# Kernel tuning notes

Measured on AMD Instinct MI355X. Metric: run time of the kernel, lower is better.

## Reference

```python
import jax, jax.numpy as jnp
import numpy as np

N = 50000; E = 800000; T = 800000; G = 64
H = 128; IEMB = 128; BAS = 8; NS = 4; NR = 6; OEH = 128; OUT = 1; NB = 4; CUT = 5.0


def envelope(x):
    # exponent=5 -> p=6: 1/x + a*x^5 + b*x^6 + c*x^7 with a=-28, b=48, c=-21
    return 1.0 / x - 28.0 * x**5 + 48.0 * x**6 - 21.0 * x**7


def setup_inputs() -> dict:
    key = jax.random.key(0)
    ks = iter(jax.random.split(key, 80))
    def w(shape, s=0.1):
        return jax.random.normal(next(ks), shape, dtype=jnp.float32) * s
    inp = {}
    inp['z'] = jax.random.randint(next(ks), (N,), 0, 100, dtype=jnp.int32)
    inp['dist'] = jax.random.uniform(next(ks), (E,), jnp.float32, 0.05, 1.0)
    inp['dist_trip'] = jax.random.uniform(next(ks), (T,), jnp.float32, 0.05, 1.0)
    inp['angle'] = jax.random.uniform(next(ks), (T,), jnp.float32, -1.0, 1.0)
    inp['edge_index'] = jax.random.randint(next(ks), (2, E), 0, N, dtype=jnp.int32)
    inp['triplets'] = jax.random.randint(next(ks), (T, 3), 0, N, dtype=jnp.int32)
    inp['batch'] = jnp.sort(jax.random.randint(next(ks), (N,), 0, G, dtype=jnp.int32))
    inp['atom_table'] = w((100, H), 1.0)
    inp['rbf_freq'] = jnp.arange(1, NR + 1, dtype=jnp.float32) * jnp.float32(np.pi)
    inp['sbf_freq'] = jnp.arange(1, NR + 1, dtype=jnp.float32) * jnp.float32(np.pi)
    inp['emb_w1'] = w((NR, IEMB)); inp['emb_b1'] = w((IEMB,), 0.01)
    inp['emb_w2'] = w((IEMB, H)); inp['emb_b2'] = w((H,), 0.01)
    inp['iw_rbf1'] = w((NB, NR, BAS)); inp['iw_rbf2'] = w((NB, BAS, H))
    inp['iw_sbf1'] = w((NB, NS * NR, BAS)); inp['iw_sbf2'] = w((NB, BAS, IEMB))
    inp['iw_t1'] = w((NB, H, IEMB)); inp['iw_t2'] = w((NB, IEMB, H)); inp['ib_t2'] = w((NB, H), 0.01)
    inp['iw_up'] = w((NB, H, H)); inp['ib_up'] = w((NB, H), 0.01)
    inp['iw_down'] = w((NB, H, H)); inp['ib_down'] = w((NB, H), 0.01)
    inp['ow_rbf'] = w((NB + 1, NR, H))
    inp['ow0'] = w((NB + 1, H, OEH)); inp['ob0'] = w((NB + 1, OEH), 0.01)
    inp['ow1'] = w((NB + 1, OEH, OEH)); inp['ob1'] = w((NB + 1, OEH), 0.01)
    inp['ow2'] = w((NB + 1, OEH, OUT)); inp['ob2'] = w((NB + 1, OUT), 0.01)
    return inp


def _forward(atom_table, rbf_freq, sbf_freq, emb_w1, emb_b1, emb_w2, emb_b2,
             iw_rbf1, iw_rbf2, iw_sbf1, iw_sbf2, iw_t1, iw_t2, ib_t2,
             iw_up, ib_up, iw_down, ib_down, ow_rbf, ow0, ob0, ow1, ob1, ow2, ob2,
             dist, dist_trip, angle, z, edge_index, triplets, batch):
    row, col = edge_index[0], edge_index[1]
    j_idx = triplets[:, 1]
    # radial basis for edges: [E, NR]
    d = dist[:, None] / CUT
    rbf_e = envelope(d) * jnp.sin(rbf_freq * d)
    # spherical basis for triplets: [T, NS*NR]
    dt = dist_trip[:, None] / CUT
    rbf_t = envelope(dt) * jnp.sin(sbf_freq * dt)
    a = angle[:, None]
    sph = jnp.concatenate([jnp.ones_like(a), a, 0.5 * (3 * a**2 - 1), 0.5 * (5 * a**3 - 3 * a)], axis=-1)
    sbf_t = (rbf_t[:, None, :] * sph[:, :, None]).reshape(a.shape[0], -1)

    x = atom_table[z]  # [N, H]
    # EmbeddingBlock: edge msg from rbf only, scattered to col
    e = jax.nn.silu(rbf_e @ emb_w1 + emb_b1) @ emb_w2 + emb_b2
    x = x + jax.ops.segment_sum(e, col, num_segments=N)

    def out_block(k, x):
        rbf_emb = rbf_e @ ow_rbf[k]            # [E, H]
        h = jax.ops.segment_sum(x[row] * rbf_emb, col, num_segments=N)
        h = jax.nn.silu(h @ ow0[k] + ob0[k])
        h = jax.nn.silu(h @ ow1[k] + ob1[k])
        return h @ ow2[k] + ob2[k]             # [N, OUT]

    P = out_block(0, x)
    for b in range(NB):
        x_up = x @ iw_up[b] + ib_up[b]
        x_down = x @ iw_down[b] + ib_down[b]
        rbf_emb = jax.nn.silu(rbf_e @ iw_rbf1[b]) @ iw_rbf2[b]      # [E, H]
        x_edge = x_up[row] * rbf_emb                                  # [E, H]
        sbf_emb = jax.nn.silu(sbf_t @ iw_sbf1[b]) @ iw_sbf2[b]      # [T, H]
        t = jax.nn.silu(x_down @ iw_t1[b]) @ iw_t2[b] + ib_t2[b]     # [N, H]
        # original: for each triplet i, x_edge += t[j]*sbf_emb[i] (broadcast over all edges)
        extra = jnp.sum(t[j_idx] * sbf_emb, axis=0)                   # [H]
        x_edge = x_edge + extra
        x = x + jax.ops.segment_sum(x_edge, col, num_segments=N)
        P = P + out_block(b + 1, x)

    counts = jax.ops.segment_sum(jnp.ones((x.shape[0],), jnp.float32), batch, num_segments=G)
    pooled = jax.ops.segment_sum(P, batch, num_segments=G) / jnp.maximum(counts, 1.0)[:, None]
    return pooled  # [G, OUT]


def reference(z, dist, dist_trip, angle, edge_index, triplets, batch, atom_table, rbf_freq, sbf_freq,
              emb_w1, emb_b1, emb_w2, emb_b2, iw_rbf1, iw_rbf2, iw_sbf1, iw_sbf2, iw_t1, iw_t2, ib_t2,
              iw_up, ib_up, iw_down, ib_down, ow_rbf, ow0, ob0, ow1, ob1, ow2, ob2):
    return _forward(atom_table, rbf_freq, sbf_freq, emb_w1, emb_b1, emb_w2, emb_b2,
                    iw_rbf1, iw_rbf2, iw_sbf1, iw_sbf2, iw_t1, iw_t2, ib_t2,
                    iw_up, ib_up, iw_down, ib_down, ow_rbf, ow0, ob0, ow1, ob1, ow2, ob2,
                    dist, dist_trip, angle, z, edge_index, triplets, batch)
```

## Files before the change

kernel.cpp:

```cpp
#include <hip/hip_runtime.h>
#include <hip/hip_fp16.h>

#define N_ 50000
#define E_ 800000
#define T_ 800000
#define G_ 64
#define H_ 128

#define NBK 782
#define NSB (NBK * 8)
#define CAPS 512

typedef __attribute__((ext_vector_type(8))) short bf16x8;
typedef __attribute__((ext_vector_type(4))) float f32x4;
typedef _Float16 f16x2 __attribute__((ext_vector_type(2)));

__device__ __forceinline__ float siluf(float v) {
    return __fdividef(v, 1.0f + __expf(-v));
}

__device__ __forceinline__ unsigned short f2bf(float f) {
    unsigned int u = __float_as_uint(f);
    u += 0x7fffu + ((u >> 16) & 1u);
    return (unsigned short)(u >> 16);
}
__device__ __forceinline__ unsigned int f2bf2(float a, float b) {
    return (unsigned int)f2bf(a) | ((unsigned int)f2bf(b) << 16);
}
__device__ __forceinline__ float bf2f(unsigned short h) {
    return __uint_as_float(((unsigned int)h) << 16);
}
__device__ __forceinline__ float2 bf2x2(unsigned int p) {
    return make_float2(__uint_as_float(p << 16), __uint_as_float(p & 0xffff0000u));
}
__device__ __forceinline__ float fdot2f(f16x2 a, f16x2 b, float c) {
    return __builtin_amdgcn_fdot2(a, b, c, false);
}

__global__ __launch_bounds__(256) void k_bucket(const int* __restrict__ ecol,
                                                const int* __restrict__ trip,
                                                int* bcntE, unsigned int* __restrict__ ebkt, int* __restrict__ degE,
                                                int* bcntT, unsigned int* __restrict__ tbkt, int* __restrict__ degT) {
    int i = blockIdx.x * 256 + threadIdx.x;
    int r = blockIdx.x & 7;
    if (i < E_) {
        int col = ecol[i];
        int sb = (col >> 6) * 8 + r;
        int pos = atomicAdd(&bcntE[sb], 1);
        if (pos < CAPS) {
            ebkt[(size_t)sb * CAPS + pos] = ((unsigned int)i << 6) | (unsigned int)(col & 63);
            atomicAdd(&degE[col], 1);
        }
    }
    int t = i - E_;
    if (t >= 0 && t < T_) {
        int j = trip[3 * t + 1];
        int sb = (j >> 6) * 8 + r;
        int pos = atomicAdd(&bcntT[sb], 1);
        if (pos < CAPS) {
            tbkt[(size_t)sb * CAPS + pos] = ((unsigned int)t << 6) | (unsigned int)(j & 63);
            atomicAdd(&degT[j], 1);
        }
    }
}

__global__ __launch_bounds__(1024) void k_scan2(const int* __restrict__ degE, int* rowptrE, int* curE,
                                                const int* __restrict__ degT, int* rowptrT, int* curT, int n) {
    const int* deg = (blockIdx.x == 0) ? degE : degT;
    int* rowptr = (blockIdx.x == 0) ? rowptrE : rowptrT;
    int* cur = (blockIdx.x == 0) ? curE : curT;
    __shared__ int wsum[16];
    __shared__ int s_carry;
    int tid = threadIdx.x, lane = tid & 63, w = tid >> 6;
    if (tid == 0) s_carry = 0;
    __syncthreads();
    for (int base = 0; base < n; base += 1024) {
        int i = base + tid;
        int v = (i < n) ? deg[i] : 0;
        int incl = v;
        #pragma unroll
        for (int s = 1; s < 64; s <<= 1) {
            int t = __shfl_up(incl, (unsigned)s, 64);
            if (lane >= s) incl += t;
        }
        if (lane == 63) wsum[w] = incl;
        __syncthreads();
        int carry0 = s_carry;
        int wexcl = 0;
        for (int j = 0; j < w; ++j) wexcl += wsum[j];
        int excl = carry0 + wexcl + (incl - v);
        if (i < n) { rowptr[i] = excl; cur[i] = excl; }
        __syncthreads();
        if (tid == 1023) s_carry = carry0 + wexcl + incl;
        __syncthreads();
    }
    if (tid == 0) rowptr[n] = s_carry;
}

__global__ __launch_bounds__(256) void k_place(const int* __restrict__ bcntE, const unsigned int* __restrict__ ebkt,
                                               const int* __restrict__ erow, const float* __restrict__ dist,
                                               int* curE, int* __restrict__ slist, float* __restrict__ distS,
                                               const int* __restrict__ bcntT, const unsigned int* __restrict__ tbkt,
                                               const float* __restrict__ dist_trip, const float* __restrict__ angle,
                                               int* curT, float2* __restrict__ tpay) {
    int b = blockIdx.x;
    bool isE = b < NBK;
    if (!isE) b -= NBK;
    int tid = threadIdx.x;
    if (isE) {
        for (int s = 0; s < 8; ++s) {
            int sb = b * 8 + s;
            int nb = min(bcntE[sb], CAPS);
            for (int i = tid; i < nb; i += 256) {
                unsigned int rec = ebkt[(size_t)sb * CAPS + i];
                int e = (int)(rec >> 6);
                int col = b * 64 + (int)(rec & 63u);
                int pos = atomicAdd(&curE[col], 1);
                slist[pos] = erow[e];
                distS[pos] = dist[e];
            }
        }
    } else {
        for (int s = 0; s < 8; ++s) {
            int sb = b * 8 + s;
            int nb = min(bcntT[sb], CAPS);
            for (int i = tid; i < nb; i += 256) {
                unsigned int rec = tbkt[(size_t)sb * CAPS + i];
                int t = (int)(rec >> 6);
                int col = b * 64 + (int)(rec & 63u);
                int pos = atomicAdd(&curT[col], 1);
                tpay[pos] = make_float2(dist_trip[t], angle[t]);
            }
        }
    }
}

__global__ __launch_bounds__(256) void k_wprep(const float* __restrict__ emb_w2, const float* __restrict__ iw_down,
                                               const float* __restrict__ iw_t1, const float* __restrict__ iw_t2,
                                               const float* __restrict__ iw_up, const float* __restrict__ ow0,
                                               const float* __restrict__ ow1, unsigned short* __restrict__ Wt) {
    int mat = blockIdx.x >> 3;
    int part = blockIdx.x & 7;
    const float* src;
    if (mat == 0) src = emb_w2;
    else if (mat < 5) src = iw_down + (size_t)(mat - 1) * 16384;
    else if (mat < 9) src = iw_t1 + (size_t)(mat - 5) * 16384;
    else if (mat < 13) src = iw_t2 + (size_t)(mat - 9) * 16384;
    else if (mat < 17) src = iw_up + (size_t)(mat - 13) * 16384;
    else if (mat < 22) src = ow0 + (size_t)(mat - 17) * 16384;
    else src = ow1 + (size_t)(mat - 22) * 16384;
    unsigned short* dst = Wt + (size_t)mat * 16384;
    int base = part * 2048;
    for (int i = base + threadIdx.x; i < base + 2048; i += 256) {
        int k = i >> 7, n = i & 127;
        dst[n * 128 + k] = f2bf(src[i]);
    }
}

__global__ __launch_bounds__(256) void k_geom(const float* __restrict__ distS,
                                              const float* __restrict__ freq, const float* __restrict__ iw_rbf1,
                                              float* __restrict__ rbfS, __half* __restrict__ s8all, int n) {
    __shared__ float W1s[4][48];
    int tid = threadIdx.x;
    if (tid < 192) W1s[tid / 48][tid % 48] = iw_rbf1[tid];
    __syncthreads();
    int p = blockIdx.x * 256 + tid;
    if (p >= n) return;
    float d = distS[p] * 0.2f;
    float d2 = d * d, d4 = d2 * d2, d5 = d4 * d;
    float env = __fdividef(1.0f, d) - 28.0f * d5 + 48.0f * d5 * d - 21.0f * d5 * d2;
    float rb[6];
    #pragma unroll
    for (int r = 0; r < 6; ++r) {
        rb[r] = env * __sinf(freq[r] * d);
        rbfS[(size_t)p * 6 + r] = rb[r];
    }
    #pragma unroll
    for (int b = 0; b < 4; ++b) {
        __half out[8];
        #pragma unroll
        for (int k = 0; k < 8; ++k) {
            float u = 0.f;
            #pragma unroll
            for (int r = 0; r < 6; ++r) u += rb[r] * W1s[b][r * 8 + k];
            out[k] = __float2half(siluf(u));
        }
        *(uint4*)&s8all[((size_t)b * n + p) * 8] = *(uint4*)out;
    }
}

__global__ __launch_bounds__(256) void k_basis(const float2* __restrict__ tpay,
                                               const float* __restrict__ sfreq, __half* __restrict__ basis, int n) {
    int t = blockIdx.x * 256 + threadIdx.x;
    if (t >= n) return;
    float2 da = tpay[t];
    float d = da.x * 0.2f;
    float a = da.y;
    float d2 = d * d, d4 = d2 * d2, d5 = d4 * d;
    float env = __fdividef(1.0f, d) - 28.0f * d5 + 48.0f * d5 * d - 21.0f * d5 * d2;
    float rb[6];
    #pragma unroll
    for (int r = 0; r < 6; ++r) rb[r] = env * __sinf(sfreq[r] * d);
    float sph[4];
    sph[0] = 1.0f; sph[1] = a; sph[2] = 1.5f * a * a - 0.5f; sph[3] = 2.5f * a * a * a - 1.5f * a;
    __half out[24];
    #pragma unroll
    for (int s = 0; s < 4; ++s)
        #pragma unroll
        for (int r = 0; r < 6; ++r) out[s * 6 + r] = __float2half(sph[s] * rb[r]);
    uint4* dst = (uint4*)(basis + (size_t)t * 24);
    dst[0] = ((uint4*)out)[0];
    dst[1] = ((uint4*)out)[1];
    dst[2] = ((uint4*)out)[2];
}

__global__ __launch_bounds__(256) void k_sv4(const int* __restrict__ rowptrT, const __half* __restrict__ basis,
                                             const float* __restrict__ iw_sbf1, float* __restrict__ SV4, int n) {
    int wave = threadIdx.x >> 6, lane = threadIdx.x & 63;
    int node = blockIdx.x * 8 + wave * 2 + (lane >> 5);
    int sub = lane & 31;
    int blk = sub >> 3, k = sub & 7;
    if (node >= n) return;
    const float* W1 = iw_sbf1 + blk * 192;
    f16x2 w[12];
    #pragma unroll
    for (int j = 0; j < 12; ++j) {
        f16x2 t;
        t.x = (_Float16)W1[(2 * j) * 8 + k];
        t.y = (_Float16)W1[(2 * j + 1) * 8 + k];
        w[j] = t;
    }
    float acc = 0.f;
    int p0 = rowptrT[node], p1 = rowptrT[node + 1];
    for (int p = p0; p < p1; ++p) {
        union { uint4 q[3]; f16x2 h[12]; } bs;
        const uint4* bp = (const uint4*)(basis + (size_t)p * 24);
        bs.q[0] = bp[0]; bs.q[1] = bp[1]; bs.q[2] = bp[2];
        float u = 0.f;
        #pragma unroll
        for (int j = 0; j < 12; ++j) u = fdot2f(bs.h[j], w[j], u);
        acc += siluf(u);
    }
    SV4[((size_t)blk * n + node) * 8 + k] = acc;
}

__global__ __launch_bounds__(256) void k_init_x(const float* __restrict__ atab, const int* __restrict__ z,
                                                unsigned short* __restrict__ xh, int n) {
    int t = blockIdx.x * 256 + threadIdx.x;
    if (t >= n * 16) return;
    int node = t >> 4, q = t & 15;
    const float4* a4 = (const float4*)atab;
    float4 v0 = a4[(size_t)z[node] * 32 + q * 2];
    float4 v1 = a4[(size_t)z[node] * 32 + q * 2 + 1];
    uint4 pk;
    pk.x = f2bf2(v0.x, v0.y);
    pk.y = f2bf2(v0.z, v0.w);
    pk.z = f2bf2(v1.x, v1.y);
    pk.w = f2bf2(v1.z, v1.w);
    ((uint4*)xh)[t] = pk;
}

__global__ __launch_bounds__(256) void k_embS(const int* __restrict__ rowptr, const float* __restrict__ rbfS,
                                              const float* __restrict__ w1, const float* __restrict__ b1,
                                              unsigned short* __restrict__ SSh, int n) {
    int node = blockIdx.x * 4 + (threadIdx.x >> 6);
    int lane = threadIdx.x & 63;
    if (node >= n) return;
    int c = lane * 2;
    float wc0[6], wc1[6];
    #pragma unroll
    for (int r = 0; r < 6; ++r) { wc0[r] = w1[r * 128 + c]; wc1[r] = w1[r * 128 + c + 1]; }
    float bb0 = b1[c], bb1 = b1[c + 1];
    float a0 = 0.f, a1 = 0.f;
    int p0 = rowptr[node], p1 = rowptr[node + 1];
    for (int p = p0; p < p1; ++p) {
        const float2* r2 = (const float2*)&rbfS[(size_t)p * 6];
        float2 ra = r2[0], rbx = r2[1], rc = r2[2];
        float u0 = bb0 + ra.x * wc0[0] + ra.y * wc0[1] + rbx.x * wc0[2] + rbx.y * wc0[3] + rc.x * wc0[4] + rc.y * wc0[5];
        float u1 = bb1 + ra.x * wc1[0] + ra.y * wc1[1] + rbx.x * wc1[2] + rbx.y * wc1[3] + rc.x * wc1[4] + rc.y * wc1[5];
        a0 += siluf(u0);
        a1 += siluf(u1);
    }
    *(unsigned int*)&SSh[(size_t)node * 128 + c] = f2bf2(a0, a1);
}

template <int BIAS_MODE, bool SILU, bool ACCBF, bool ABF, bool WF32, bool WBF>
__global__ __launch_bounds__(256, 4) void k_gemm_mfma(const void* __restrict__ Ap,
                                                      const unsigned short* __restrict__ Wt,
                                                      const float* __restrict__ bias, const int* __restrict__ deg,
                                                      float* __restrict__ C, unsigned short* __restrict__ Ch, int M) {
    int tid = threadIdx.x;
    int wave = tid >> 6, lane = tid & 63;
    int m15 = lane & 15, quad = lane >> 4;
    int row0 = blockIdx.x * 64 + wave * 16;
    int arow = row0 + m15;
    if (arow > M - 1) arow = M - 1;

    f32x4 acc[8];
    #pragma unroll
    for (int nt = 0; nt < 8; ++nt) acc[nt] = (f32x4){0.f, 0.f, 0.f, 0.f};

    #pragma unroll
    for (int kt = 0; kt < 4; ++kt) {
        int ks = kt * 32 + quad * 8;
        bf16x8 av;
        if constexpr (ABF) {
            av = *(const bf16x8*)((const unsigned short*)Ap + (size_t)arow * 128 + ks);
        } else {
            const float* Arow = (const float*)Ap + (size_t)arow * 128;
            float4 a0 = *(const float4*)(Arow + ks);
            float4 a1 = *(const float4*)(Arow + ks + 4);
            union { bf16x8 v; unsigned int u[4]; } af;
            af.u[0] = f2bf2(a0.x, a0.y);
            af.u[1] = f2bf2(a0.z, a0.w);
            af.u[2] = f2bf2(a1.x, a1.y);
            af.u[3] = f2bf2(a1.z, a1.w);
            av = af.v;
        }
        #pragma unroll
        for (int nt = 0; nt < 8; ++nt) {
            bf16x8 bf = *(const bf16x8*)(Wt + (size_t)(nt * 16 + m15) * 128 + ks);
            acc[nt] = __builtin_amdgcn_mfma_f32_16x16x32_bf16(av, bf, acc[nt], 0, 0, 0);
        }
    }

    #pragma unroll
    for (int nt = 0; nt < 8; ++nt) {
        int col = nt * 16 + m15;
        float bc = 0.f;
        if constexpr (BIAS_MODE != 0) bc = bias[col];
        #pragma unroll
        for (int reg = 0; reg < 4; ++reg) {
            int row = row0 + quad * 4 + reg;
            if (row < M) {
                float v = acc[nt][reg];
                if constexpr (BIAS_MODE == 1) v += bc;
                if constexpr (BIAS_MODE == 2) v += bc * (float)deg[row];
                if constexpr (SILU) v = siluf(v);
                if constexpr (ACCBF) v += bf2f(Ch[(size_t)row * 128 + col]);
                if constexpr (WF32) C[(size_t)row * 128 + col] = v;
                if constexpr (WBF) Ch[(size_t)row * 128 + col] = f2bf(v);
            }
        }
    }
}

template <int PACC>
__global__ __launch_bounds__(256, 4) void k_out_mlp(const unsigned short* __restrict__ hB,
                                                    const unsigned short* __restrict__ W0t, const float* __restrict__ b0,
                                                    const unsigned short* __restrict__ W1t, const float* __restrict__ b1,
                                                    const float* __restrict__ w2col, const float* __restrict__ ob2p,
                                                    float* __restrict__ Pout, int M) {
    __shared__ unsigned short lds[4][16 * 136];
    int tid = threadIdx.x;
    int wave = tid >> 6, lane = tid & 63;
    int m15 = lane & 15, quad = lane >> 4;
    int row0 = blockIdx.x * 64 + wave * 16;
    int arow = row0 + m15;
    if (arow > M - 1) arow = M - 1;
    unsigned short* L = lds[wave];

    f32x4 acc[8];
    #pragma unroll
    for (int nt = 0; nt < 8; ++nt) acc[nt] = (f32x4){0.f, 0.f, 0.f, 0.f};
    #pragma unroll
    for (int kt = 0; kt < 4; ++kt) {
        int ks = kt * 32 + quad * 8;
        bf16x8 av = *(const bf16x8*)(hB + (size_t)arow * 128 + ks);
        #pragma unroll
        for (int nt = 0; nt < 8; ++nt) {
            bf16x8 bf = *(const bf16x8*)(W0t + (size_t)(nt * 16 + m15) * 128 + ks);
            acc[nt] = __builtin_amdgcn_mfma_f32_16x16x32_bf16(av, bf, acc[nt], 0, 0, 0);
        }
    }
    #pragma unroll
    for (int nt = 0; nt < 8; ++nt) {
        int col = nt * 16 + m15;
        float bc = b0[col];
        #pragma unroll
        for (int reg = 0; reg < 4; ++reg)
            L[(quad * 4 + reg) * 136 + col] = f2bf(siluf(acc[nt][reg] + bc));
    }
    __syncthreads();

    #pragma unroll
    for (int nt = 0; nt < 8; ++nt) acc[nt] = (f32x4){0.f, 0.f, 0.f, 0.f};
    #pragma unroll
    for (int kt = 0; kt < 4; ++kt) {
        int ks = kt * 32 + quad * 8;
        bf16x8 av = *(const bf16x8*)(L + m15 * 136 + ks);
        #pragma unroll
        for (int nt = 0; nt < 8; ++nt) {
            bf16x8 bf = *(const bf16x8*)(W1t + (size_t)(nt * 16 + m15) * 128 + ks);
            acc[nt] = __builtin_amdgcn_mfma_f32_16x16x32_bf16(av, bf, acc[nt], 0, 0, 0);
        }
    }
    float w2c[8], pp[4];
    #pragma unroll
    for (int nt = 0; nt < 8; ++nt) w2c[nt] = w2col[nt * 16 + m15];
    #pragma unroll
    for (int reg = 0; reg < 4; ++reg) pp[reg] = 0.f;
    #pragma unroll
    for (int nt = 0; nt < 8; ++nt) {
        float bc = b1[nt * 16 + m15];
        #pragma unroll
        for (int reg = 0; reg < 4; ++reg)
            pp[reg] += siluf(acc[nt][reg] + bc) * w2c[nt];
    }
    #pragma unroll
    for (int reg = 0; reg < 4; ++reg) {
        float s = pp[reg];
        s += __shfl_xor(s, 1, 64);
        s += __shfl_xor(s, 2, 64);
        s += __shfl_xor(s, 4, 64);
        s += __shfl_xor(s, 8, 64);
        if (m15 == 0) {
            int row = row0 + quad * 4 + reg;
            if (row < M) {
                float r = s + ob2p[0];
                if constexpr (PACC == 2) r += Pout[row];
                Pout[row] = r;
            }
        }
    }
}

__global__ __launch_bounds__(256, 4) void k_block_mlp(const unsigned short* __restrict__ xh,
                                                      const unsigned short* __restrict__ Wd, const float* __restrict__ bd,
                                                      const unsigned short* __restrict__ Wt1,
                                                      const unsigned short* __restrict__ Wt2, const float* __restrict__ bt2,
                                                      const unsigned short* __restrict__ Wup, const float* __restrict__ bup,
                                                      const float* __restrict__ SV, const float* __restrict__ W2,
                                                      float* __restrict__ extra,
                                                      unsigned short* __restrict__ xuph, int M) {
    __shared__ union {
        unsigned short h[4][16 * 136];
        float f[64 * 132];
    } sm;
    int tid = threadIdx.x;
    int wave = tid >> 6, lane = tid & 63;
    int m15 = lane & 15, quad = lane >> 4;
    int row0 = blockIdx.x * 64 + wave * 16;
    int arow = row0 + m15;
    if (arow > M - 1) arow = M - 1;
    unsigned short* L = sm.h[wave];

    f32x4 accD[8], accU[8];
    #pragma unroll
    for (int nt = 0; nt < 8; ++nt) { accD[nt] = (f32x4){0.f, 0.f, 0.f, 0.f}; accU[nt] = (f32x4){0.f, 0.f, 0.f, 0.f}; }
    #pragma unroll
    for (int kt = 0; kt < 4; ++kt) {
        int ks = kt * 32 + quad * 8;
        bf16x8 av = *(const bf16x8*)(xh + (size_t)arow * 128 + ks);
        #pragma unroll
        for (int nt = 0; nt < 8; ++nt) {
            bf16x8 bd_ = *(const bf16x8*)(Wd + (size_t)(nt * 16 + m15) * 128 + ks);
            accD[nt] = __builtin_amdgcn_mfma_f32_16x16x32_bf16(av, bd_, accD[nt], 0, 0, 0);
            bf16x8 bu_ = *(const bf16x8*)(Wup + (size_t)(nt * 16 + m15) * 128 + ks);
            accU[nt] = __builtin_amdgcn_mfma_f32_16x16x32_bf16(av, bu_, accU[nt], 0, 0, 0);
        }
    }
    #pragma unroll
    for (int nt = 0; nt < 8; ++nt) {
        int col = nt * 16 + m15;
        float bcu = bup[col], bcd = bd[col];
        #pragma unroll
        for (int reg = 0; reg < 4; ++reg) {
            int row = row0 + quad * 4 + reg;
            if (row < M) xuph[(size_t)row * 128 + col] = f2bf(accU[nt][reg] + bcu);
            L[(quad * 4 + reg) * 136 + col] = f2bf(accD[nt][reg] + bcd);
        }
    }
    __syncthreads();

    #pragma unroll
    for (int nt = 0; nt < 8; ++nt) accD[nt] = (f32x4){0.f, 0.f, 0.f, 0.f};
    #pragma unroll
    for (int kt = 0; kt < 4; ++kt) {
        int ks = kt * 32 + quad * 8;
        bf16x8 av = *(const bf16x8*)(L + m15 * 136 + ks);
        #pragma unroll
        for (int nt = 0; nt < 8; ++nt) {
            bf16x8 bf = *(const bf16x8*)(Wt1 + (size_t)(nt * 16 + m15) * 128 + ks);
            accD[nt] = __builtin_amdgcn_mfma_f32_16x16x32_bf16(av, bf, accD[nt], 0, 0, 0);
        }
    }
    __syncthreads();
    #pragma unroll
    for (int nt = 0; nt < 8; ++nt) {
        int col = nt * 16 + m15;
        #pragma unroll
        for (int reg = 0; reg < 4; ++reg)
            L[(quad * 4 + reg) * 136 + col] = f2bf(siluf(accD[nt][reg]));
    }
    __syncthreads();

    #pragma unroll
    for (int nt = 0; nt < 8; ++nt) accD[nt] = (f32x4){0.f, 0.f, 0.f, 0.f};
    #pragma unroll
    for (int kt = 0; kt < 4; ++kt) {
        int ks = kt * 32 + quad * 8;
        bf16x8 av = *(const bf16x8*)(L + m15 * 136 + ks);
        #pragma unroll
        for (int nt = 0; nt < 8; ++nt) {
            bf16x8 bf = *(const bf16x8*)(Wt2 + (size_t)(nt * 16 + m15) * 128 + ks);
            accD[nt] = __builtin_amdgcn_mfma_f32_16x16x32_bf16(av, bf, accD[nt], 0, 0, 0);
        }
    }
    __syncthreads();
    #pragma unroll
    for (int nt = 0; nt < 8; ++nt) {
        int col = nt * 16 + m15;
        float bc = bt2[col];
        #pragma unroll
        for (int reg = 0; reg < 4; ++reg) {
            int lr = wave * 16 + quad * 4 + reg;
            sm.f[lr * 132 + col] = accD[nt][reg] + bc;
        }
    }
    __syncthreads();

    int col = tid & 127, half = tid >> 7;
    float acc8[8];
    #pragma unroll
    for (int k = 0; k < 8; ++k) acc8[k] = 0.f;
    int rmax = M - blockIdx.x * 64;
    if (rmax > 64) rmax = 64;
    for (int rr = half; rr < rmax; rr += 2) {
        float t = sm.f[rr * 132 + col];
        const float4* sv4 = (const float4*)&SV[(size_t)(blockIdx.x * 64 + rr) * 8];
        float4 s0 = sv4[0], s1 = sv4[1];
        acc8[0] += t * s0.x; acc8[1] += t * s0.y; acc8[2] += t * s0.z; acc8[3] += t * s0.w;
        acc8[4] += t * s1.x; acc8[5] += t * s1.y; acc8[6] += t * s1.z; acc8[7] += t * s1.w;
    }
    float e = 0.f;
    #pragma unroll
    for (int k = 0; k < 8; ++k) e += acc8[k] * W2[k * 128 + col];
    __syncthreads();
    sm.f[tid] = e;
    __syncthreads();
    if (tid < 128) atomicAdd(&extra[col], sm.f[tid] + sm.f[tid + 128]);
}

__global__ __launch_bounds__(256) void k_out_gather(const int* __restrict__ rowptr, const int* __restrict__ slist,
                                                    const float* __restrict__ rbfS,
                                                    const unsigned short* __restrict__ xh,
                                                    const float* __restrict__ wrbf,
                                                    unsigned short* __restrict__ hB, int n) {
    int node = blockIdx.x * 4 + (threadIdx.x >> 6);
    int lane = threadIdx.x & 63;
    if (node >= n) return;
    int c = lane * 2;
    float wc0[6], wc1[6];
    #pragma unroll
    for (int r = 0; r < 6; ++r) { wc0[r] = wrbf[r * 128 + c]; wc1[r] = wrbf[r * 128 + c + 1]; }
    float a0 = 0.f, a1 = 0.f;
    int p0 = rowptr[node], p1 = rowptr[node + 1];
    int p = p0;
    for (; p + 4 <= p1; p += 4) {
        int s0 = slist[p], s1 = slist[p + 1], s2 = slist[p + 2], s3 = slist[p + 3];
        float2 rb[4][3];
        #pragma unroll
        for (int u = 0; u < 4; ++u) {
            const float2* r2 = (const float2*)&rbfS[(size_t)(p + u) * 6];
            rb[u][0] = r2[0]; rb[u][1] = r2[1]; rb[u][2] = r2[2];
        }
        unsigned int xv0 = *(const unsigned int*)&xh[(size_t)s0 * 128 + c];
        unsigned int xv1 = *(const unsigned int*)&xh[(size_t)s1 * 128 + c];
        unsigned int xv2 = *(const unsigned int*)&xh[(size_t)s2 * 128 + c];
        unsigned int xv3 = *(const unsigned int*)&xh[(size_t)s3 * 128 + c];
        #pragma unroll
        for (int u = 0; u < 4; ++u) {
            float e0 = rb[u][0].x * wc0[0] + rb[u][0].y * wc0[1] + rb[u][1].x * wc0[2] +
                       rb[u][1].y * wc0[3] + rb[u][2].x * wc0[4] + rb[u][2].y * wc0[5];
            float e1 = rb[u][0].x * wc1[0] + rb[u][0].y * wc1[1] + rb[u][1].x * wc1[2] +
                       rb[u][1].y * wc1[3] + rb[u][2].x * wc1[4] + rb[u][2].y * wc1[5];
            float2 xf = bf2x2((u == 0) ? xv0 : (u == 1) ? xv1 : (u == 2) ? xv2 : xv3);
            a0 += xf.x * e0;
            a1 += xf.y * e1;
        }
    }
    for (; p < p1; ++p) {
        int src = slist[p];
        const float2* r2 = (const float2*)&rbfS[(size_t)p * 6];
        float2 ra = r2[0], rbx = r2[1], rc = r2[2];
        float e0 = ra.x * wc0[0] + ra.y * wc0[1] + rbx.x * wc0[2] + rbx.y * wc0[3] + rc.x * wc0[4] + rc.y * wc0[5];
        float e1 = ra.x * wc1[0] + ra.y * wc1[1] + rbx.x * wc1[2] + rbx.y * wc1[3] + rc.x * wc1[4] + rc.y * wc1[5];
        float2 xf = bf2x2(*(const unsigned int*)&xh[(size_t)src * 128 + c]);
        a0 += xf.x * e0;
        a1 += xf.y * e1;
    }
    *(unsigned int*)&hB[(size_t)node * 128 + c] = f2bf2(a0, a1);
}

__global__ __launch_bounds__(256) void k_interact(const int* __restrict__ rowptr, const int* __restrict__ slist,
                                                  const __half* __restrict__ s8, const float* __restrict__ W2,
                                                  const float* __restrict__ extra,
                                                  const unsigned short* __restrict__ xuph,
                                                  unsigned short* __restrict__ xh, int n) {
    int node = blockIdx.x * 4 + (threadIdx.x >> 6);
    int lane = threadIdx.x & 63;
    if (node >= n) return;
    int c = lane * 2;
    f16x2 w2a[4], w2b[4];
    #pragma unroll
    for (int j = 0; j < 4; ++j) {
        f16x2 wa, wb;
        wa.x = (_Float16)W2[(2 * j) * 128 + c];
        wa.y = (_Float16)W2[(2 * j + 1) * 128 + c];
        wb.x = (_Float16)W2[(2 * j) * 128 + c + 1];
        wb.y = (_Float16)W2[(2 * j + 1) * 128 + c + 1];
        w2a[j] = wa;
        w2b[j] = wb;
    }
    int p0 = rowptr[node], p1 = rowptr[node + 1];
    float cntf = (float)(p1 - p0);
    float a0 = cntf * extra[c], a1 = cntf * extra[c + 1];
    int p = p0;
    for (; p + 4 <= p1; p += 4) {
        int s0 = slist[p], s1 = slist[p + 1], s2 = slist[p + 2], s3 = slist[p + 3];
        uint4 sv[4];
        #pragma unroll
        for (int u = 0; u < 4; ++u) sv[u] = *(const uint4*)(s8 + (size_t)(p + u) * 8);
        unsigned int xv0 = *(const unsigned int*)&xuph[(size_t)s0 * 128 + c];
        unsigned int xv1 = *(const unsigned int*)&xuph[(size_t)s1 * 128 + c];
        unsigned int xv2 = *(const unsigned int*)&xuph[(size_t)s2 * 128 + c];
        unsigned int xv3 = *(const unsigned int*)&xuph[(size_t)s3 * 128 + c];
        #pragma unroll
        for (int u = 0; u < 4; ++u) {
            union { uint4 q; f16x2 h[4]; } s;
            s.q = sv[u];
            float e0 = fdot2f(s.h[0], w2a[0], 0.f);
            e0 = fdot2f(s.h[1], w2a[1], e0);
            e0 = fdot2f(s.h[2], w2a[2], e0);
            e0 = fdot2f(s.h[3], w2a[3], e0);
            float e1 = fdot2f(s.h[0], w2b[0], 0.f);
            e1 = fdot2f(s.h[1], w2b[1], e1);
            e1 = fdot2f(s.h[2], w2b[2], e1);
            e1 = fdot2f(s.h[3], w2b[3], e1);
            float2 xf = bf2x2((u == 0) ? xv0 : (u == 1) ? xv1 : (u == 2) ? xv2 : xv3);
            a0 += xf.x * e0;
            a1 += xf.y * e1;
        }
    }
    for (; p < p1; ++p) {
        int src = slist[p];
        float2 xf = bf2x2(*(const unsigned int*)&xuph[(size_t)src * 128 + c]);
        union { uint4 q; f16x2 h[4]; } s;
        s.q = *(const uint4*)(s8 + (size_t)p * 8);
        float e0 = fdot2f(s.h[0], w2a[0], 0.f);
        e0 = fdot2f(s.h[1], w2a[1], e0);
        e0 = fdot2f(s.h[2], w2a[2], e0);
        e0 = fdot2f(s.h[3], w2a[3], e0);
        float e1 = fdot2f(s.h[0], w2b[0], 0.f);
        e1 = fdot2f(s.h[1], w2b[1], e1);
        e1 = fdot2f(s.h[2], w2b[2], e1);
        e1 = fdot2f(s.h[3], w2b[3], e1);
        a0 += xf.x * e0;
        a1 += xf.y * e1;
    }
    unsigned int cur = *(unsigned int*)&xh[(size_t)node * 128 + c];
    float2 xc = bf2x2(cur);
    *(unsigned int*)&xh[(size_t)node * 128 + c] = f2bf2(xc.x + a0, xc.y + a1);
}

__global__ __launch_bounds__(256) void k_pool(const float* __restrict__ P, const int* __restrict__ batch,
                                              float* __restrict__ pool, float* __restrict__ cnt, int n) {
    int i = blockIdx.x * 256 + threadIdx.x;
    int lane = threadIdx.x & 63;
    int b = (i < n) ? batch[i] : -1;
    float p = (i < n) ? P[i] : 0.f;
    int b0 = __shfl(b, 0, 64);
    int b63 = __shfl(b, 63, 64);
    if (b0 == b63 && b0 >= 0) {
        float s = p;
        #pragma unroll
        for (int off = 32; off > 0; off >>= 1) s += __shfl_xor(s, off, 64);
        if (lane == 0) {
            atomicAdd(&pool[b0], s);
            atomicAdd(&cnt[b0], 64.0f);
        }
    } else {
        if (i < n) {
            atomicAdd(&pool[b], p);
            atomicAdd(&cnt[b], 1.0f);
        }
    }
}

__global__ __launch_bounds__(64) void k_final(const float* __restrict__ pool, const float* __restrict__ cnt,
                                              float* __restrict__ out) {
    int g = threadIdx.x;
    if (g < G_) out[g] = __fdividef(pool[g], fmaxf(cnt[g], 1.0f));
}

extern "C" void kernel_launch(void* const* d_in, const int* in_sizes, int n_in,
                              void* d_out, int out_size, void* d_ws, size_t ws_size,
                              hipStream_t stream) {
    (void)in_sizes; (void)n_in; (void)out_size; (void)ws_size;
    const int* z = (const int*)d_in[0];
    const float* dist = (const float*)d_in[1];
    const float* dist_trip = (const float*)d_in[2];
    const float* angle = (const float*)d_in[3];
    const int* edge_index = (const int*)d_in[4];
    const int* triplets = (const int*)d_in[5];
    const int* batch = (const int*)d_in[6];
    const float* atom_table = (const float*)d_in[7];
    const float* rbf_freq = (const float*)d_in[8];
    const float* sbf_freq = (const float*)d_in[9];
    const float* emb_w1 = (const float*)d_in[10];
    const float* emb_b1 = (const float*)d_in[11];
    const float* emb_w2 = (const float*)d_in[12];
    const float* emb_b2 = (const float*)d_in[13];
    const float* iw_rbf1 = (const float*)d_in[14];
    const float* iw_rbf2 = (const float*)d_in[15];
    const float* iw_sbf1 = (const float*)d_in[16];
    const float* iw_sbf2 = (const float*)d_in[17];
    const float* iw_t1 = (const float*)d_in[18];
    const float* iw_t2 = (const float*)d_in[19];
    const float* ib_t2 = (const float*)d_in[20];
    const float* iw_up = (const float*)d_in[21];
    const float* ib_up = (const float*)d_in[22];
    const float* iw_down = (const float*)d_in[23];
    const float* ib_down = (const float*)d_in[24];
    const float* ow_rbf = (const float*)d_in[25];
    const float* ow0 = (const float*)d_in[26];
    const float* ob0 = (const float*)d_in[27];
    const float* ow1 = (const float*)d_in[28];
    const float* ob1 = (const float*)d_in[29];
    const float* ow2 = (const float*)d_in[30];
    const float* ob2 = (const float*)d_in[31];

    const int* erow = edge_index;
    const int* ecol = edge_index + E_;

    float* ws = (float*)d_ws;
    float* bufA = ws;
    float* bufB = bufA + (size_t)N_ * H_;
    float* P = bufB + (size_t)N_ * H_;
    float* rbfS = P + N_;
    float* SV4 = rbfS + (size_t)E_ * 6;
    float* extra4 = SV4 + (size_t)4 * N_ * 8;
    float* pool = extra4 + 512;
    float* cnt = pool + G_;
    int* bcntE = (int*)(cnt + G_);
    int* bcntT = bcntE + NSB;
    int* degE = bcntT + NSB;
    int* degT = degE + N_;
    int* rowptr = degT + N_;
    int* curE = rowptr + N_ + 1;
    int* curT = curE + N_;
    int* slist = curT + N_;
    int* rowptrT = slist + E_;
    float* distS = (float*)(rowptrT + N_ + 1);
    uintptr_t tp = (uintptr_t)(distS + E_);
    tp = (tp + 7) & ~(uintptr_t)7;
    float2* tpay = (float2*)tp;
    __half* s8all = (__half*)(tpay + T_);
    __half* basis = s8all + (size_t)4 * E_ * 8;
    unsigned short* xh = (unsigned short*)(basis + (size_t)T_ * 24);
    unsigned short* xuph = xh + (size_t)N_ * H_;
    unsigned short* Wt = xuph + (size_t)N_ * H_;
    unsigned short* hB = (unsigned short*)bufB;

    unsigned int* ebkt = (unsigned int*)s8all;
    unsigned int* tbkt = ebkt + (size_t)NSB * CAPS;

    const int EG = (E_ + 255) / 256;
    const int TG = (T_ + 255) / 256;
    const int ETG = (E_ + T_ + 255) / 256;
    const int NG4 = (N_ + 3) / 4;
    const int GEMMG = (N_ + 63) / 64;

    hipMemsetAsync(extra4, 0, (512 + 2 * G_ + 2 * NSB + 2 * N_) * sizeof(float), stream);
    k_wprep<<<27 * 8, 256, 0, stream>>>(emb_w2, iw_down, iw_t1, iw_t2, iw_up, ow0, ow1, Wt);
    k_bucket<<<ETG, 256, 0, stream>>>(ecol, triplets, bcntE, ebkt, degE, bcntT, tbkt, degT);
    k_scan2<<<2, 1024, 0, stream>>>(degE, rowptr, curE, degT, rowptrT, curT, N_);
    k_place<<<2 * NBK, 256, 0, stream>>>(bcntE, ebkt, erow, dist, curE, slist, distS,
                                         bcntT, tbkt, dist_trip, angle, curT, tpay);

    k_geom<<<EG, 256, 0, stream>>>(distS, rbf_freq, iw_rbf1, rbfS, s8all, E_);
    k_basis<<<TG, 256, 0, stream>>>(tpay, sbf_freq, basis, T_);
    k_sv4<<<(N_ + 7) / 8, 256, 0, stream>>>(rowptrT, basis, iw_sbf1, SV4, N_);
    k_init_x<<<(N_ * 16 + 255) / 256, 256, 0, stream>>>(atom_table, z, xh, N_);

    k_embS<<<NG4, 256, 0, stream>>>(rowptr, rbfS, emb_w1, emb_b1, (unsigned short*)bufA, N_);
    k_gemm_mfma<2, false, true, true, false, true><<<GEMMG, 256, 0, stream>>>(
        bufA, Wt, emb_b2, degE, nullptr, xh, N_);

    auto out_block = [&](int k, bool first) {
        k_out_gather<<<NG4, 256, 0, stream>>>(rowptr, slist, rbfS, xh,
                                              ow_rbf + (size_t)k * 6 * 128, hB, N_);
        if (first)
            k_out_mlp<1><<<GEMMG, 256, 0, stream>>>(hB, Wt + (size_t)(17 + k) * 16384, ob0 + k * 128,
                                                    Wt + (size_t)(22 + k) * 16384, ob1 + k * 128,
                                                    ow2 + k * 128, ob2 + k, P, N_);
        else
            k_out_mlp<2><<<GEMMG, 256, 0, stream>>>(hB, Wt + (size_t)(17 + k) * 16384, ob0 + k * 128,
                                                    Wt + (size_t)(22 + k) * 16384, ob1 + k * 128,
                                                    ow2 + k * 128, ob2 + k, P, N_);
    };

    out_block(0, true);

    for (int b = 0; b < 4; ++b) {
        k_block_mlp<<<GEMMG, 256, 0, stream>>>(xh,
                                               Wt + (size_t)(1 + b) * 16384, ib_down + b * 128,
                                               Wt + (size_t)(5 + b) * 16384,
                                               Wt + (size_t)(9 + b) * 16384, ib_t2 + b * 128,
                                               Wt + (size_t)(13 + b) * 16384, ib_up + b * 128,
                                               SV4 + (size_t)b * N_ * 8,
                                               iw_sbf2 + (size_t)b * 1024,
                                               extra4 + b * 128,
                                               xuph, N_);
        k_interact<<<NG4, 256, 0, stream>>>(rowptr, slist, s8all + (size_t)b * E_ * 8,
                                            iw_rbf2 + (size_t)b * 1024, extra4 + b * 128,
                                            xuph, xh, N_);
        out_block(b + 1, false);
    }

    k_pool<<<(N_ + 255) / 256, 256, 0, stream>>>(P, batch, pool, cnt, N_);
    k_final<<<1, 64, 0, stream>>>(pool, cnt, (float*)d_out);
}
```

Baseline: 1.701 ms.

## Rebuild CSR construction with block-local histograms and per-bucket scans

The bucketing kernel now gives each block a 4096-element chunk and builds a shared-memory histogram per bucket, so each block issues one global atomic per bucket instead of one per element. The global per-node degree count and the 50k-element serial scan are replaced by a small scan over 782 bucket totals. The place kernel then computes per-column offsets in shared memory and writes rowptr itself, and the GEMM derives degree from rowptr differences. This cuts global atomic traffic and the long single-block scan, at the cost of extra LDS atomics and a second pass over the buckets in place.

Measured after the change: 1.508 ms. -11.4%, faster.

```diff
diff --git a/kernel.cpp b/kernel.cpp
--- a/kernel.cpp
+++ b/kernel.cpp
@@ -10,6 +10,9 @@
 #define NBK 782
 #define NSB (NBK * 8)
 #define CAPS 512
+#define CHUNK 4096
+#define EB ((E_ + CHUNK - 1) / CHUNK)
+#define TB ((T_ + CHUNK - 1) / CHUNK)
 
 typedef __attribute__((ext_vector_type(8))) short bf16x8;
 typedef __attribute__((ext_vector_type(4))) float f32x4;
@@ -39,97 +42,137 @@
 
 __global__ __launch_bounds__(256) void k_bucket(const int* __restrict__ ecol,
                                                 const int* __restrict__ trip,
-                                                int* bcntE, unsigned int* __restrict__ ebkt, int* __restrict__ degE,
-                                                int* bcntT, unsigned int* __restrict__ tbkt, int* __restrict__ degT) {
-    int i = blockIdx.x * 256 + threadIdx.x;
-    int r = blockIdx.x & 7;
-    if (i < E_) {
-        int col = ecol[i];
-        int sb = (col >> 6) * 8 + r;
-        int pos = atomicAdd(&bcntE[sb], 1);
-        if (pos < CAPS) {
-            ebkt[(size_t)sb * CAPS + pos] = ((unsigned int)i << 6) | (unsigned int)(col & 63);
-            atomicAdd(&degE[col], 1);
-        }
-    }
-    int t = i - E_;
-    if (t >= 0 && t < T_) {
-        int j = trip[3 * t + 1];
-        int sb = (j >> 6) * 8 + r;
-        int pos = atomicAdd(&bcntT[sb], 1);
-        if (pos < CAPS) {
-            tbkt[(size_t)sb * CAPS + pos] = ((unsigned int)t << 6) | (unsigned int)(j & 63);
-            atomicAdd(&degT[j], 1);
-        }
-    }
-}
-
-__global__ __launch_bounds__(1024) void k_scan2(const int* __restrict__ degE, int* rowptrE, int* curE,
-                                                const int* __restrict__ degT, int* rowptrT, int* curT, int n) {
-    const int* deg = (blockIdx.x == 0) ? degE : degT;
-    int* rowptr = (blockIdx.x == 0) ? rowptrE : rowptrT;
-    int* cur = (blockIdx.x == 0) ? curE : curT;
+                                                int* bcntE, unsigned int* __restrict__ ebkt,
+                                                int* bcntT, unsigned int* __restrict__ tbkt) {
+    __shared__ int hist[NBK];
+    __shared__ int bbase[NBK];
+    int blk = blockIdx.x;
+    bool isE = blk < EB;
+    int ebase = (isE ? blk : blk - EB) * CHUNK;
+    const int nElem = isE ? E_ : T_;
+    int r = blk & 7;
+    int* bcnt = isE ? bcntE : bcntT;
+    unsigned int* bkt = isE ? ebkt : tbkt;
+    int tid = threadIdx.x;
+
+    for (int i = tid; i < NBK; i += 256) hist[i] = 0;
+    __syncthreads();
+
+    int cols[16];
+    #pragma unroll
+    for (int u = 0; u < 16; ++u) {
+        int idx = ebase + u * 256 + tid;
+        int c = -1;
+        if (idx < nElem) c = isE ? ecol[idx] : trip[3 * idx + 1];
+        cols[u] = c;
+        if (c >= 0) atomicAdd(&hist[c >> 6], 1);
+    }
+    __syncthreads();
+
+    for (int b = tid; b < NBK; b += 256) {
+        int c = hist[b];
+        bbase[b] = c ? atomicAdd(&bcnt[b * 8 + r], c) : 0;
+        hist[b] = 0;
+    }
+    __syncthreads();
+
+    #pragma unroll
+    for (int u = 0; u < 16; ++u) {
+        int c = cols[u];
+        if (c >= 0) {
+            int bk = c >> 6;
+            int off = atomicAdd(&hist[bk], 1);
+            int pos = bbase[bk] + off;
+            if (pos < CAPS) {
+                int idx = ebase + u * 256 + tid;
+                bkt[(size_t)(bk * 8 + r) * CAPS + pos] =
+                    ((unsigned int)idx << 6) | (unsigned int)(c & 63);
+            }
+        }
+    }
+}
+
+__global__ __launch_bounds__(1024) void k_scanB(const int* __restrict__ bcntE, int* bktbaseE,
+                                                const int* __restrict__ bcntT, int* bktbaseT) {
+    const int* bcnt = (blockIdx.x == 0) ? bcntE : bcntT;
+    int* bb = (blockIdx.x == 0) ? bktbaseE : bktbaseT;
+    int tid = threadIdx.x, lane = tid & 63, w = tid >> 6;
     __shared__ int wsum[16];
-    __shared__ int s_carry;
-    int tid = threadIdx.x, lane = tid & 63, w = tid >> 6;
-    if (tid == 0) s_carry = 0;
-    __syncthreads();
-    for (int base = 0; base < n; base += 1024) {
-        int i = base + tid;
-        int v = (i < n) ? deg[i] : 0;
-        int incl = v;
-        #pragma unroll
-        for (int s = 1; s < 64; s <<= 1) {
-            int t = __shfl_up(incl, (unsigned)s, 64);
-            if (lane >= s) incl += t;
-        }
-        if (lane == 63) wsum[w] = incl;
-        __syncthreads();
-        int carry0 = s_carry;
-        int wexcl = 0;
-        for (int j = 0; j < w; ++j) wexcl += wsum[j];
-        int excl = carry0 + wexcl + (incl - v);
-        if (i < n) { rowptr[i] = excl; cur[i] = excl; }
-        __syncthreads();
-        if (tid == 1023) s_carry = carry0 + wexcl + incl;
-        __syncthreads();
-    }
-    if (tid == 0) rowptr[n] = s_carry;
+    int v = 0;
+    if (tid < NBK) {
+        #pragma unroll
+        for (int s = 0; s < 8; ++s) v += min(bcnt[tid * 8 + s], CAPS);
+    }
+    int incl = v;
+    #pragma unroll
+    for (int s = 1; s < 64; s <<= 1) {
+        int t = __shfl_up(incl, (unsigned)s, 64);
+        if (lane >= s) incl += t;
+    }
+    if (lane == 63) wsum[w] = incl;
+    __syncthreads();
+    int wexcl = 0;
+    for (int j = 0; j < w; ++j) wexcl += wsum[j];
+    if (tid < NBK) bb[tid] = wexcl + incl - v;
 }
 
 __global__ __launch_bounds__(256) void k_place(const int* __restrict__ bcntE, const unsigned int* __restrict__ ebkt,
                                                const int* __restrict__ erow, const float* __restrict__ dist,
-                                               int* curE, int* __restrict__ slist, float* __restrict__ distS,
+                                               const int* __restrict__ bktbaseE, int* __restrict__ rowptrE,
+                                               int* __restrict__ slist, float* __restrict__ distS,
                                                const int* __restrict__ bcntT, const unsigned int* __restrict__ tbkt,
                                                const float* __restrict__ dist_trip, const float* __restrict__ angle,
-                                               int* curT, float2* __restrict__ tpay) {
+                                               const int* __restrict__ bktbaseT, int* __restrict__ rowptrT,
+                                               float2* __restrict__ tpay) {
     int b = blockIdx.x;
     bool isE = b < NBK;
     if (!isE) b -= NBK;
     int tid = threadIdx.x;
-    if (isE) {
-        for (int s = 0; s < 8; ++s) {
-            int sb = b * 8 + s;
-            int nb = min(bcntE[sb], CAPS);
-            for (int i = tid; i < nb; i += 256) {
-                unsigned int rec = ebkt[(size_t)sb * CAPS + i];
-                int e = (int)(rec >> 6);
-                int col = b * 64 + (int)(rec & 63u);
-                int pos = atomicAdd(&curE[col], 1);
+    __shared__ int ccnt[64];
+    __shared__ int cbase[64];
+    __shared__ int nb[8];
+    if (tid < 64) ccnt[tid] = 0;
+    const int* bcnt = isE ? bcntE : bcntT;
+    const unsigned int* bkt = isE ? ebkt : tbkt;
+    if (tid < 8) nb[tid] = min(bcnt[b * 8 + tid], CAPS);
+    __syncthreads();
+    for (int s = 0; s < 8; ++s) {
+        int n = nb[s];
+        const unsigned int* src = bkt + (size_t)(b * 8 + s) * CAPS;
+        for (int i = tid; i < n; i += 256) atomicAdd(&ccnt[src[i] & 63u], 1);
+    }
+    __syncthreads();
+    if (tid < 64) {
+        int v = ccnt[tid];
+        int incl = v;
+        #pragma unroll
+        for (int s = 1; s < 64; s <<= 1) {
+            int t = __shfl_up(incl, (unsigned)s, 64);
+            if (tid >= s) incl += t;
+        }
+        int base = (isE ? bktbaseE : bktbaseT)[b];
+        int excl = base + incl - v;
+        cbase[tid] = excl;
+        int col = b * 64 + tid;
+        int* rp = isE ? rowptrE : rowptrT;
+        if (col <= N_) rp[col] = excl;
+        ccnt[tid] = 0;
+    }
+    __syncthreads();
+    for (int s = 0; s < 8; ++s) {
+        int n = nb[s];
+        const unsigned int* src = bkt + (size_t)(b * 8 + s) * CAPS;
+        for (int i = tid; i < n; i += 256) {
+            unsigned int rec = src[i];
+            int c = (int)(rec & 63u);
+            int e = (int)(rec >> 6);
+            int off = atomicAdd(&ccnt[c], 1);
+            int pos = cbase[c] + off;
+            if (isE) {
                 slist[pos] = erow[e];
                 distS[pos] = dist[e];
-            }
-        }
-    } else {
-        for (int s = 0; s < 8; ++s) {
-            int sb = b * 8 + s;
-            int nb = min(bcntT[sb], CAPS);
-            for (int i = tid; i < nb; i += 256) {
-                unsigned int rec = tbkt[(size_t)sb * CAPS + i];
-                int t = (int)(rec >> 6);
-                int col = b * 64 + (int)(rec & 63u);
-                int pos = atomicAdd(&curT[col], 1);
-                tpay[pos] = make_float2(dist_trip[t], angle[t]);
+            } else {
+                tpay[pos] = make_float2(dist_trip[e], angle[e]);
             }
         }
     }
@@ -287,7 +330,7 @@
 template <int BIAS_MODE, bool SILU, bool ACCBF, bool ABF, bool WF32, bool WBF>
 __global__ __launch_bounds__(256, 4) void k_gemm_mfma(const void* __restrict__ Ap,
                                                       const unsigned short* __restrict__ Wt,
-                                                      const float* __restrict__ bias, const int* __restrict__ deg,
+                                                      const float* __restrict__ bias, const int* __restrict__ rp,
                                                       float* __restrict__ C, unsigned short* __restrict__ Ch, int M) {
     int tid = threadIdx.x;
     int wave = tid >> 6, lane = tid & 63;
@@ -335,7 +378,7 @@
             if (row < M) {
                 float v = acc[nt][reg];
                 if constexpr (BIAS_MODE == 1) v += bc;
-                if constexpr (BIAS_MODE == 2) v += bc * (float)deg[row];
+                if constexpr (BIAS_MODE == 2) v += bc * (float)(rp[row + 1] - rp[row]);
                 if constexpr (SILU) v = siluf(v);
                 if constexpr (ACCBF) v += bf2f(Ch[(size_t)row * 128 + col]);
                 if constexpr (WF32) C[(size_t)row * 128 + col] = v;
@@ -745,14 +788,12 @@
     float* cnt = pool + G_;
     int* bcntE = (int*)(cnt + G_);
     int* bcntT = bcntE + NSB;
-    int* degE = bcntT + NSB;
-    int* degT = degE + N_;
-    int* rowptr = degT + N_;
-    int* curE = rowptr + N_ + 1;
-    int* curT = curE + N_;
-    int* slist = curT + N_;
-    int* rowptrT = slist + E_;
-    float* distS = (float*)(rowptrT + N_ + 1);
+    int* bktbaseE = bcntT + NSB;
+    int* bktbaseT = bktbaseE + NBK;
+    int* rowptr = bktbaseT + NBK;
+    int* rowptrT = rowptr + N_ + 1;
+    int* slist = rowptrT + N_ + 1;
+    float* distS = (float*)(slist + E_);
     uintptr_t tp = (uintptr_t)(distS + E_);
     tp = (tp + 7) & ~(uintptr_t)7;
     float2* tpay = (float2*)tp;
@@ -768,16 +809,15 @@
 
     const int EG = (E_ + 255) / 256;
     const int TG = (T_ + 255) / 256;
-    const int ETG = (E_ + T_ + 255) / 256;
     const int NG4 = (N_ + 3) / 4;
     const int GEMMG = (N_ + 63) / 64;
 
-    hipMemsetAsync(extra4, 0, (512 + 2 * G_ + 2 * NSB + 2 * N_) * sizeof(float), stream);
+    hipMemsetAsync(extra4, 0, (512 + 2 * G_ + 2 * NSB) * sizeof(float), stream);
     k_wprep<<<27 * 8, 256, 0, stream>>>(emb_w2, iw_down, iw_t1, iw_t2, iw_up, ow0, ow1, Wt);
-    k_bucket<<<ETG, 256, 0, stream>>>(ecol, triplets, bcntE, ebkt, degE, bcntT, tbkt, degT);
-    k_scan2<<<2, 1024, 0, stream>>>(degE, rowptr, curE, degT, rowptrT, curT, N_);
-    k_place<<<2 * NBK, 256, 0, stream>>>(bcntE, ebkt, erow, dist, curE, slist, distS,
-                                         bcntT, tbkt, dist_trip, angle, curT, tpay);
+    k_bucket<<<EB + TB, 256, 0, stream>>>(ecol, triplets, bcntE, ebkt, bcntT, tbkt);
+    k_scanB<<<2, 1024, 0, stream>>>(bcntE, bktbaseE, bcntT, bktbaseT);
+    k_place<<<2 * NBK, 256, 0, stream>>>(bcntE, ebkt, erow, dist, bktbaseE, rowptr, slist, distS,
+                                         bcntT, tbkt, dist_trip, angle, bktbaseT, rowptrT, tpay);
 
     k_geom<<<EG, 256, 0, stream>>>(distS, rbf_freq, iw_rbf1, rbfS, s8all, E_);
     k_basis<<<TG, 256, 0, stream>>>(tpay, sbf_freq, basis, T_);
@@ -786,7 +826,7 @@
 
     k_embS<<<NG4, 256, 0, stream>>>(rowptr, rbfS, emb_w1, emb_b1, (unsigned short*)bufA, N_);
     k_gemm_mfma<2, false, true, true, false, true><<<GEMMG, 256, 0, stream>>>(
-        bufA, Wt, emb_b2, degE, nullptr, xh, N_);
+        bufA, Wt, emb_b2, rowptr, nullptr, xh, N_);
 
     auto out_block = [&](int k, bool first) {
         k_out_gather<<<NG4, 256, 0, stream>>>(rowptr, slist, rbfS, xh,
```
